# Kernel tuning notes

Hardware: AMD Instinct MI355X
Metric: run time of the kernel (lower is better)

The kernel has to match this reference:

```python
import jax, jax.numpy as jnp
import numpy as np
from jax import lax

B, P, ENC, DEC, ATT, EMB, V, L = 64, 196, 2048, 512, 512, 512, 10000, 30


def setup_inputs() -> dict:
    key = jax.random.key(0)
    ks = jax.random.split(key, 24)
    s = 0.02
    encoder_out = jax.random.normal(ks[0], (B, P, ENC), dtype=jnp.float32)
    encoded_captions = jax.random.randint(ks[1], (B, L), 0, V, dtype=jnp.int64)
    caption_lengths = jax.random.randint(ks[2], (B, 1), 2, L + 1, dtype=jnp.int64)
    # ensure max decode length == L-1 (matches torch max(decode_lengths))
    caption_lengths = caption_lengths.at[0, 0].set(L)
    p = lambda k, sh: jax.random.normal(k, sh, dtype=jnp.float32) * s
    return {
        "encoder_out": encoder_out,
        "encoded_captions": encoded_captions,
        "caption_lengths": caption_lengths,
        "W_enc": p(ks[3], (ATT, ENC)), "b_enc": jnp.zeros((ATT,), jnp.float32),
        "W_dec": p(ks[4], (ATT, DEC)), "b_dec": jnp.zeros((ATT,), jnp.float32),
        "w_full": p(ks[5], (ATT,)), "b_full": jnp.zeros((), jnp.float32),
        "emb_table": jax.random.uniform(ks[6], (V, EMB), jnp.float32, -0.1, 0.1),
        "W_ih": p(ks[7], (4 * DEC, EMB + ENC)), "b_ih": jnp.zeros((4 * DEC,), jnp.float32),
        "W_hh": p(ks[8], (4 * DEC, DEC)), "b_hh": jnp.zeros((4 * DEC,), jnp.float32),
        "W_init_h": p(ks[9], (DEC, ENC)), "b_init_h": jnp.zeros((DEC,), jnp.float32),
        "W_init_c": p(ks[10], (DEC, ENC)), "b_init_c": jnp.zeros((DEC,), jnp.float32),
        "W_beta": p(ks[11], (ENC, DEC)), "b_beta": jnp.zeros((ENC,), jnp.float32),
        "W_fc": jax.random.uniform(ks[12], (V, DEC), jnp.float32, -0.1, 0.1),
        "b_fc": jnp.zeros((V,), jnp.float32),
    }


def reference(encoder_out, encoded_captions, caption_lengths,
              W_enc, b_enc, W_dec, b_dec, w_full, b_full, emb_table,
              W_ih, b_ih, W_hh, b_hh, W_init_h, b_init_h, W_init_c, b_init_c,
              W_beta, b_beta, W_fc, b_fc):
    lengths = caption_lengths[:, 0]
    sort_ind = jnp.argsort(-lengths)  # descending, stable
    enc = encoder_out[sort_ind]            # [B,P,ENC]
    caps = encoded_captions[sort_ind]      # [B,L]
    dec_lens = lengths[sort_ind] - 1       # [B]
    T = caps.shape[1] - 1

    embs = emb_table[caps]                 # [B,L,EMB]
    mean_enc = enc.mean(axis=1)
    h0 = mean_enc @ W_init_h.T + b_init_h
    c0 = mean_enc @ W_init_c.T + b_init_c
    # encoder attention projection is h-independent: compute once
    att1 = jnp.einsum('bpe,ae->bpa', enc, W_enc) + b_enc  # [B,P,ATT]

    def step(carry, xs):
        h, c = carry
        emb_t, mask_t = xs  # [B,EMB], [B] bool
        att2 = h @ W_dec.T + b_dec                              # [B,ATT]
        e = jax.nn.relu(att1 + att2[:, None, :]) @ w_full + b_full  # [B,P]
        alpha = jax.nn.softmax(e, axis=1)
        awe = jnp.einsum('bp,bpe->be', alpha, enc)              # [B,ENC]
        gate = jax.nn.sigmoid(h @ W_beta.T + b_beta)
        awe = gate * awe
        x = jnp.concatenate([emb_t, awe], axis=1)               # [B,EMB+ENC]
        gates = x @ W_ih.T + b_ih + h @ W_hh.T + b_hh           # [B,4D]
        i, f, g, o = jnp.split(gates, 4, axis=1)
        i, f, o = jax.nn.sigmoid(i), jax.nn.sigmoid(f), jax.nn.sigmoid(o)
        g = jnp.tanh(g)
        c_new = f * c + i * g
        h_new = o * jnp.tanh(c_new)
        preds = h_new @ W_fc.T + b_fc                           # [B,V]  (dropout: eval/identity)
        m = mask_t[:, None].astype(preds.dtype)
        return (h_new, c_new), (preds * m, alpha * m)

    mask = jnp.arange(T)[:, None] < dec_lens[None, :]           # [T,B]
    embs_t = jnp.swapaxes(embs[:, :T], 0, 1)                    # [T,B,EMB]
    _, (preds, alphas) = lax.scan(step, (h0, c0), (embs_t, mask))
    predictions = jnp.swapaxes(preds, 0, 1)                     # [B,T,V]
    alphas = jnp.swapaxes(alphas, 0, 1)                         # [B,T,P]
    return predictions, alphas, caps, dec_lens, sort_ind
```

## Files before the change

### kernel.cpp

```cpp
#include <hip/hip_runtime.h>
#include <hip/hip_bf16.h>
#include <math.h>
#include <float.h>

#define BDIM   64
#define PDIM   196
#define ENC    2048
#define DECD   512
#define ATTD   512
#define EMBD   512
#define VOC    10000
#define LCAP   30
#define TSTEPS 29

typedef __attribute__((ext_vector_type(8))) short s8v;
typedef __attribute__((ext_vector_type(4))) float f4v;

__device__ __forceinline__ float sigf(float x) { return 1.0f / (1.0f + expf(-x)); }
__device__ __forceinline__ float bf2f(ushort u) { return __uint_as_float(((uint)u) << 16); }

__global__ void sort_kernel(const int* __restrict__ cap_len,
                            const int* __restrict__ caps,
                            int* __restrict__ sort_ind,
                            int* __restrict__ dec_lens,
                            int* __restrict__ caps_s,
                            float* __restrict__ out_caps,
                            float* __restrict__ out_dlen,
                            float* __restrict__ out_sind) {
    int i = threadIdx.x;
    __shared__ int len[BDIM];
    len[i] = cap_len[i];
    __syncthreads();
    int li = len[i];
    int r = 0;
    for (int j = 0; j < BDIM; ++j) {
        int lj = len[j];
        if (lj > li || (lj == li && j < i)) ++r;
    }
    sort_ind[r] = i;
    dec_lens[r] = li - 1;
    out_sind[r] = (float)i;
    out_dlen[r] = (float)(li - 1);
    for (int tt = 0; tt < LCAP; ++tt) {
        int v = caps[i * LCAP + tt];
        caps_s[r * LCAP + tt] = v;
        out_caps[r * LCAP + tt] = (float)v;
    }
}

__global__ __launch_bounds__(256) void conv_enc_kernel(const float* __restrict__ enc,
                                                       const int* __restrict__ sort_ind,
                                                       __hip_bfloat16* __restrict__ enc_s,
                                                       float* __restrict__ mean_enc) {
    int b = blockIdx.y, tid = threadIdx.x;
    int e = (blockIdx.x << 8) + tid;
    const float* ep = enc + (size_t)sort_ind[b] * (PDIM * ENC) + e;
    __hip_bfloat16* op = enc_s + (size_t)b * (PDIM * ENC) + e;
    float s = 0.f;
    for (int p = 0; p < PDIM; ++p) {
        float v = ep[(size_t)p * ENC];
        s += v;
        op[(size_t)p * ENC] = __float2bfloat16(v);
    }
    mean_enc[(size_t)b * ENC + e] = s * (1.0f / (float)PDIM);
}

__global__ __launch_bounds__(256) void f2b_kernel(const float* __restrict__ src,
                                                  __hip_bfloat16* __restrict__ dst, int n) {
    int i = blockIdx.x * 256 + threadIdx.x;
    if (i < n) dst[i] = __float2bfloat16(src[i]);
}

__global__ __launch_bounds__(256) void h0_kernel(const float* __restrict__ h0f,
                                                 __hip_bfloat16* __restrict__ xh) {
    int idx = blockIdx.x * 256 + threadIdx.x;
    int b = idx >> 9, j = idx & 511;
    xh[(size_t)b * 3072 + 2560 + j] = __float2bfloat16(h0f[idx]);
}

__global__ __launch_bounds__(256) void gemm32_k(
    const float* __restrict__ A, int lda,
    const float* __restrict__ W0, const float* __restrict__ bias0,
    float* __restrict__ C, int ldc, int K) {
    __shared__ float As[16][64];
    __shared__ float Ws[16][64];
    const int tid = threadIdx.x;
    const int tx = tid & 15, ty = tid >> 4;
    const int bn0 = blockIdx.x * 64;
    const int lr = tid >> 2;
    const int lk = (tid & 3) << 2;
    const float* Arow = A + (size_t)lr * lda;
    const int wn = bn0 + lr;
    float acc[4][4];
#pragma unroll
    for (int i = 0; i < 4; ++i)
#pragma unroll
        for (int j = 0; j < 4; ++j) acc[i][j] = 0.f;
    for (int k0 = 0; k0 < K; k0 += 16) {
        float4 av = *(const float4*)(Arow + k0 + lk);
        float4 wv = *(const float4*)(W0 + (size_t)wn * K + k0 + lk);
        __syncthreads();
        As[lk + 0][lr] = av.x; As[lk + 1][lr] = av.y;
        As[lk + 2][lr] = av.z; As[lk + 3][lr] = av.w;
        Ws[lk + 0][lr] = wv.x; Ws[lk + 1][lr] = wv.y;
        Ws[lk + 2][lr] = wv.z; Ws[lk + 3][lr] = wv.w;
        __syncthreads();
#pragma unroll
        for (int kk = 0; kk < 16; ++kk) {
            const float4 a = *(const float4*)&As[kk][ty << 2];
            const float4 w = *(const float4*)&Ws[kk][tx << 2];
            acc[0][0] += a.x * w.x; acc[0][1] += a.x * w.y; acc[0][2] += a.x * w.z; acc[0][3] += a.x * w.w;
            acc[1][0] += a.y * w.x; acc[1][1] += a.y * w.y; acc[1][2] += a.y * w.z; acc[1][3] += a.y * w.w;
            acc[2][0] += a.z * w.x; acc[2][1] += a.z * w.y; acc[2][2] += a.z * w.z; acc[2][3] += a.z * w.w;
            acc[3][0] += a.w * w.x; acc[3][1] += a.w * w.y; acc[3][2] += a.w * w.z; acc[3][3] += a.w * w.w;
        }
    }
#pragma unroll
    for (int i = 0; i < 4; ++i) {
        int row = (ty << 2) + i;
#pragma unroll
        for (int j = 0; j < 4; ++j) {
            int col = bn0 + (tx << 2) + j;
            C[(size_t)row * ldc + col] = acc[i][j] + bias0[col];
        }
    }
}

enum { E_ATT1 = 0, E_GACT = 1, E_GATES = 2, E_PREDS = 3 };

template <int MF, int MODE>
__global__ __launch_bounds__(64) void mfma_gemm(
    const __hip_bfloat16* __restrict__ A, int lda,
    const __hip_bfloat16* __restrict__ W0, const __hip_bfloat16* __restrict__ W1,
    const float* __restrict__ bias0, const float* __restrict__ bias1,
    void* __restrict__ Cv, int K,
    const int* __restrict__ dec_lens, int t) {
    const int l = threadIdx.x;
    const int c16 = l & 15, kg = l >> 4;
    const int n0 = blockIdx.x * 64;
    const int m0 = blockIdx.y * (16 * MF);

    f4v acc[MF][4];
#pragma unroll
    for (int mi = 0; mi < MF; ++mi)
#pragma unroll
        for (int ni = 0; ni < 4; ++ni) acc[mi][ni] = (f4v)0.0f;

    const __hip_bfloat16* arow[MF];
#pragma unroll
    for (int mi = 0; mi < MF; ++mi)
        arow[mi] = A + (size_t)(m0 + mi * 16 + c16) * lda + kg * 8;

    const __hip_bfloat16* wrow[4];
#pragma unroll
    for (int ni = 0; ni < 4; ++ni) {
        int n = n0 + ni * 16 + c16;
        if (MODE == E_GACT)
            wrow[ni] = (n < 2048) ? W0 + (size_t)n * 512 : W1 + (size_t)(n - 2048) * 512;
        else if (MODE == E_GATES)
            wrow[ni] = W0 + (size_t)n * 2560;
        else if (MODE == E_PREDS) {
            int nn = (n < VOC) ? n : (VOC - 1);
            wrow[ni] = W0 + (size_t)nn * K;
        } else
            wrow[ni] = W0 + (size_t)n * K;
        wrow[ni] += kg * 8;
    }

    for (int k0 = 0; k0 < K; k0 += 32) {
        s8v a[MF], b[4];
#pragma unroll
        for (int mi = 0; mi < MF; ++mi)
            a[mi] = *(const s8v*)(arow[mi] + k0);
#pragma unroll
        for (int ni = 0; ni < 4; ++ni) {
            if (MODE == E_GATES && k0 >= 2560)
                b[ni] = *(const s8v*)(W1 + (size_t)(n0 + ni * 16 + c16) * 512 + (k0 - 2560) + kg * 8);
            else
                b[ni] = *(const s8v*)(wrow[ni] + k0);
        }
#pragma unroll
        for (int mi = 0; mi < MF; ++mi)
#pragma unroll
            for (int ni = 0; ni < 4; ++ni)
                acc[mi][ni] = __builtin_amdgcn_mfma_f32_16x16x32_bf16(a[mi], b[ni], acc[mi][ni], 0, 0, 0);
    }

#pragma unroll
    for (int mi = 0; mi < MF; ++mi) {
#pragma unroll
        for (int ni = 0; ni < 4; ++ni) {
#pragma unroll
            for (int i = 0; i < 4; ++i) {
                int r = m0 + mi * 16 + kg * 4 + i;
                int c = n0 + ni * 16 + c16;
                float v = acc[mi][ni][i];
                if (MODE == E_ATT1) {
                    ((__hip_bfloat16*)Cv)[(size_t)r * 512 + c] = __float2bfloat16(v + bias0[c]);
                } else if (MODE == E_GACT) {
                    float* C = (float*)Cv;
                    if (c < 2048) C[(size_t)r * 2560 + c] = sigf(v + bias0[c]);
                    else          C[(size_t)r * 2560 + c] = v + bias1[c - 2048];
                } else if (MODE == E_GATES) {
                    ((float*)Cv)[(size_t)r * 2048 + c] = v + bias0[c] + bias1[c];
                } else {
                    if (c < VOC) {
                        float o = v + bias0[c];
                        ((float*)Cv)[(size_t)r * (TSTEPS * VOC) + (size_t)t * VOC + c] =
                            (t < dec_lens[r]) ? o : 0.f;
                    }
                }
            }
        }
    }
}

__global__ __launch_bounds__(256) void att_kernel(
    const __hip_bfloat16* __restrict__ att1, const float* __restrict__ gact,
    const float* __restrict__ w_full, const float* __restrict__ b_full,
    float* __restrict__ alpha_ws, float* __restrict__ out_alphas,
    const int* __restrict__ dec_lens, int t) {
    int b = blockIdx.x;
    int tid = threadIdx.x;
    __shared__ float s_att2[ATTD];
    __shared__ float s_wf[ATTD];
    __shared__ float s_e[PDIM];
    __shared__ float red[256];

    s_att2[tid]       = gact[(size_t)b * 2560 + 2048 + tid];
    s_att2[tid + 256] = gact[(size_t)b * 2560 + 2048 + 256 + tid];
    s_wf[tid]       = w_full[tid];
    s_wf[tid + 256] = w_full[tid + 256];
    __syncthreads();

    int wv = tid >> 6, lane = tid & 63;
    const float bf = b_full[0];
    const int a0 = lane << 3;
    for (int p = wv; p < PDIM; p += 4) {
        const ushort* row = (const ushort*)att1 + ((size_t)b * PDIM + p) * ATTD + a0;
        float s = 0.f;
#pragma unroll
        for (int i = 0; i < 8; ++i) {
            float x = bf2f(row[i]) + s_att2[a0 + i];
            s += fmaxf(x, 0.f) * s_wf[a0 + i];
        }
#pragma unroll
        for (int off = 32; off; off >>= 1) s += __shfl_xor(s, off);
        if (lane == 0) s_e[p] = s + bf;
    }
    __syncthreads();

    float v = (tid < PDIM) ? s_e[tid] : -FLT_MAX;
    red[tid] = v;
    __syncthreads();
    for (int st = 128; st; st >>= 1) {
        if (tid < st) red[tid] = fmaxf(red[tid], red[tid + st]);
        __syncthreads();
    }
    float mx = red[0];
    __syncthreads();
    float ex = (tid < PDIM) ? expf(v - mx) : 0.f;
    red[tid] = ex;
    __syncthreads();
    for (int st = 128; st; st >>= 1) {
        if (tid < st) red[tid] += red[tid + st];
        __syncthreads();
    }
    float inv = 1.f / red[0];
    if (tid < PDIM) {
        float al = ex * inv;
        alpha_ws[b * PDIM + tid] = al;
        out_alphas[(size_t)b * (TSTEPS * PDIM) + (size_t)t * PDIM + tid] =
            (t < dec_lens[b]) ? al : 0.f;
    }
}

__global__ __launch_bounds__(256) void awe_kernel(
    const __hip_bfloat16* __restrict__ enc_s, const float* __restrict__ alpha_ws,
    const float* __restrict__ gact, const float* __restrict__ emb_table,
    const int* __restrict__ caps_s, __hip_bfloat16* __restrict__ xh, int t) {
    int b = blockIdx.y, tid = threadIdx.x;
    __shared__ float s_al[PDIM];
    if (tid < PDIM) s_al[tid] = alpha_ws[b * PDIM + tid];
    __syncthreads();
    int e = (blockIdx.x << 9) + (tid << 1);
    const ushort* ep = (const ushort*)enc_s + (size_t)b * (PDIM * ENC) + e;
    float a0x = 0.f, a0y = 0.f, a1x = 0.f, a1y = 0.f;
    for (int p = 0; p < PDIM; p += 2) {
        ushort2 u0 = *(const ushort2*)(ep + (size_t)p * ENC);
        ushort2 u1 = *(const ushort2*)(ep + (size_t)(p + 1) * ENC);
        float al0 = s_al[p], al1 = s_al[p + 1];
        a0x += al0 * bf2f(u0.x); a0y += al0 * bf2f(u0.y);
        a1x += al1 * bf2f(u1.x); a1y += al1 * bf2f(u1.y);
    }
    float gx = gact[(size_t)b * 2560 + e];
    float gy = gact[(size_t)b * 2560 + e + 1];
    __hip_bfloat16* xp = xh + (size_t)b * 3072 + 512 + e;
    xp[0] = __float2bfloat16((a0x + a1x) * gx);
    xp[1] = __float2bfloat16((a0y + a1y) * gy);
    if (blockIdx.x == 0) {
        int cap = caps_s[b * LCAP + t];
        int j = tid << 1;
        const float* em = emb_table + (size_t)cap * EMBD + j;
        __hip_bfloat16* xe = xh + (size_t)b * 3072 + j;
        xe[0] = __float2bfloat16(em[0]);
        xe[1] = __float2bfloat16(em[1]);
    }
}

__global__ __launch_bounds__(256) void cell_kernel(const float* __restrict__ gates,
                                                   float* __restrict__ c,
                                                   __hip_bfloat16* __restrict__ xh) {
    int idx = blockIdx.x * 256 + threadIdx.x;
    int b = idx >> 9, j = idx & 511;
    const float* g = gates + (size_t)b * 2048;
    float i_ = sigf(g[j]);
    float f_ = sigf(g[512 + j]);
    float g_ = tanhf(g[1024 + j]);
    float o_ = sigf(g[1536 + j]);
    float cn = f_ * c[idx] + i_ * g_;
    c[idx] = cn;
    xh[(size_t)b * 3072 + 2560 + j] = __float2bfloat16(o_ * tanhf(cn));
}

extern "C" void kernel_launch(void* const* d_in, const int* in_sizes, int n_in,
                              void* d_out, int out_size, void* d_ws, size_t ws_size,
                              hipStream_t stream) {
    const float* enc      = (const float*)d_in[0];
    const int*   caps     = (const int*)d_in[1];
    const int*   clen     = (const int*)d_in[2];
    const float* W_enc    = (const float*)d_in[3];
    const float* b_enc    = (const float*)d_in[4];
    const float* W_dec    = (const float*)d_in[5];
    const float* b_dec    = (const float*)d_in[6];
    const float* w_full   = (const float*)d_in[7];
    const float* b_full   = (const float*)d_in[8];
    const float* emb_tab  = (const float*)d_in[9];
    const float* W_ih     = (const float*)d_in[10];
    const float* b_ih     = (const float*)d_in[11];
    const float* W_hh     = (const float*)d_in[12];
    const float* b_hh     = (const float*)d_in[13];
    const float* W_init_h = (const float*)d_in[14];
    const float* b_init_h = (const float*)d_in[15];
    const float* W_init_c = (const float*)d_in[16];
    const float* b_init_c = (const float*)d_in[17];
    const float* W_beta   = (const float*)d_in[18];
    const float* b_beta   = (const float*)d_in[19];
    const float* W_fc     = (const float*)d_in[20];
    const float* b_fc     = (const float*)d_in[21];

    float* out_pred = (float*)d_out;
    float* out_alph = out_pred + (size_t)BDIM * TSTEPS * VOC;
    float* out_caps = out_alph + (size_t)BDIM * TSTEPS * PDIM;
    float* out_dlen = out_caps + BDIM * LCAP;
    float* out_sind = out_dlen + BDIM;

    char* p = (char*)d_ws;
    auto carve = [&](size_t bytes) { char* r = p; p += (bytes + 255) & ~(size_t)255; return r; };
    int* sort_ind = (int*)carve(64 * 4);
    int* dec_lens = (int*)carve(64 * 4);
    int* caps_s   = (int*)carve(64 * LCAP * 4);
    float* mean_e = (float*)carve((size_t)64 * ENC * 4);
    float* h0f    = (float*)carve((size_t)64 * 512 * 4);
    float* cbuf   = (float*)carve((size_t)64 * 512 * 4);
    float* gact   = (float*)carve((size_t)64 * 2560 * 4);
    float* gates  = (float*)carve((size_t)64 * 2048 * 4);
    float* alpha  = (float*)carve((size_t)64 * PDIM * 4);
    __hip_bfloat16* xh     = (__hip_bfloat16*)carve((size_t)64 * 3072 * 2);
    __hip_bfloat16* enc_s  = (__hip_bfloat16*)carve((size_t)64 * PDIM * ENC * 2);
    __hip_bfloat16* att1   = (__hip_bfloat16*)carve((size_t)64 * PDIM * 512 * 2);
    __hip_bfloat16* Wb_enc = (__hip_bfloat16*)carve((size_t)512 * 2048 * 2);
    __hip_bfloat16* Wb_bet = (__hip_bfloat16*)carve((size_t)2048 * 512 * 2);
    __hip_bfloat16* Wb_dec = (__hip_bfloat16*)carve((size_t)512 * 512 * 2);
    __hip_bfloat16* Wb_ih  = (__hip_bfloat16*)carve((size_t)2048 * 2560 * 2);
    __hip_bfloat16* Wb_hh  = (__hip_bfloat16*)carve((size_t)2048 * 512 * 2);
    __hip_bfloat16* Wb_fc  = (__hip_bfloat16*)carve((size_t)VOC * 512 * 2);

    sort_kernel<<<1, 64, 0, stream>>>(clen, caps, sort_ind, dec_lens, caps_s,
                                      out_caps, out_dlen, out_sind);
    conv_enc_kernel<<<dim3(8, 64), 256, 0, stream>>>(enc, sort_ind, enc_s, mean_e);
    f2b_kernel<<<(512 * 2048 + 255) / 256, 256, 0, stream>>>(W_enc, Wb_enc, 512 * 2048);
    f2b_kernel<<<(2048 * 512 + 255) / 256, 256, 0, stream>>>(W_beta, Wb_bet, 2048 * 512);
    f2b_kernel<<<(512 * 512 + 255) / 256, 256, 0, stream>>>(W_dec, Wb_dec, 512 * 512);
    f2b_kernel<<<(2048 * 2560 + 255) / 256, 256, 0, stream>>>(W_ih, Wb_ih, 2048 * 2560);
    f2b_kernel<<<(2048 * 512 + 255) / 256, 256, 0, stream>>>(W_hh, Wb_hh, 2048 * 512);
    f2b_kernel<<<(VOC * 512 + 255) / 256, 256, 0, stream>>>(W_fc, Wb_fc, VOC * 512);

    gemm32_k<<<dim3(8, 1), 256, 0, stream>>>(mean_e, ENC, W_init_h, b_init_h, h0f, 512, ENC);
    gemm32_k<<<dim3(8, 1), 256, 0, stream>>>(mean_e, ENC, W_init_c, b_init_c, cbuf, 512, ENC);
    h0_kernel<<<128, 256, 0, stream>>>(h0f, xh);

    mfma_gemm<2, E_ATT1><<<dim3(8, 392), 64, 0, stream>>>(
        enc_s, ENC, Wb_enc, nullptr, b_enc, nullptr, att1, ENC, nullptr, 0);

    for (int t = 0; t < TSTEPS; ++t) {
        mfma_gemm<1, E_GACT><<<dim3(40, 4), 64, 0, stream>>>(
            xh + 2560, 3072, Wb_bet, Wb_dec, b_beta, b_dec, gact, 512, nullptr, 0);
        att_kernel<<<64, 256, 0, stream>>>(att1, gact, w_full, b_full,
                                           alpha, out_alph, dec_lens, t);
        awe_kernel<<<dim3(4, 64), 256, 0, stream>>>(enc_s, alpha, gact, emb_tab,
                                                    caps_s, xh, t);
        mfma_gemm<1, E_GATES><<<dim3(32, 4), 64, 0, stream>>>(
            xh, 3072, Wb_ih, Wb_hh, b_ih, b_hh, gates, 3072, nullptr, 0);
        cell_kernel<<<128, 256, 0, stream>>>(gates, cbuf, xh);
        mfma_gemm<1, E_PREDS><<<dim3(157, 4), 64, 0, stream>>>(
            xh + 2560, 3072, Wb_fc, nullptr, b_fc, nullptr, out_pred, 512, dec_lens, t);
    }
}
```

Before: 3.467 ms.

## Fuse attention softmax with weighted encoding and specialize GEMM K at compile time

```diff
diff --git a/kernel.cpp b/kernel.cpp
--- a/kernel.cpp
+++ b/kernel.cpp
@@ -128,17 +128,17 @@
 
 enum { E_ATT1 = 0, E_GACT = 1, E_GATES = 2, E_PREDS = 3 };
 
-template <int MF, int MODE>
+template <int MF, int MODE, int KA, int KB, bool XM>
 __global__ __launch_bounds__(64) void mfma_gemm(
     const __hip_bfloat16* __restrict__ A, int lda,
     const __hip_bfloat16* __restrict__ W0, const __hip_bfloat16* __restrict__ W1,
     const float* __restrict__ bias0, const float* __restrict__ bias1,
-    void* __restrict__ Cv, int K,
+    void* __restrict__ Cv,
     const int* __restrict__ dec_lens, int t) {
     const int l = threadIdx.x;
     const int c16 = l & 15, kg = l >> 4;
-    const int n0 = blockIdx.x * 64;
-    const int m0 = blockIdx.y * (16 * MF);
+    const int n0 = (XM ? (int)blockIdx.y : (int)blockIdx.x) * 64;
+    const int m0 = (XM ? (int)blockIdx.x : (int)blockIdx.y) * (16 * MF);
 
     f4v acc[MF][4];
 #pragma unroll
@@ -151,39 +151,53 @@
     for (int mi = 0; mi < MF; ++mi)
         arow[mi] = A + (size_t)(m0 + mi * 16 + c16) * lda + kg * 8;
 
-    const __hip_bfloat16* wrow[4];
+    const __hip_bfloat16* w0r[4];
+    const __hip_bfloat16* w1r[4];
 #pragma unroll
     for (int ni = 0; ni < 4; ++ni) {
         int n = n0 + ni * 16 + c16;
-        if (MODE == E_GACT)
-            wrow[ni] = (n < 2048) ? W0 + (size_t)n * 512 : W1 + (size_t)(n - 2048) * 512;
-        else if (MODE == E_GATES)
-            wrow[ni] = W0 + (size_t)n * 2560;
-        else if (MODE == E_PREDS) {
+        if (MODE == E_GACT) {
+            w0r[ni] = (n < 2048) ? W0 + (size_t)n * 512 : W1 + (size_t)(n - 2048) * 512;
+        } else if (MODE == E_GATES) {
+            w0r[ni] = W0 + (size_t)n * (KA);
+            w1r[ni] = W1 + (size_t)n * (KB);
+        } else if (MODE == E_PREDS) {
             int nn = (n < VOC) ? n : (VOC - 1);
-            wrow[ni] = W0 + (size_t)nn * K;
-        } else
-            wrow[ni] = W0 + (size_t)n * K;
-        wrow[ni] += kg * 8;
-    }
-
-    for (int k0 = 0; k0 < K; k0 += 32) {
+            w0r[ni] = W0 + (size_t)nn * KA;
+        } else {
+            w0r[ni] = W0 + (size_t)n * KA;
+        }
+        w0r[ni] += kg * 8;
+        if (MODE == E_GATES) w1r[ni] += kg * 8;
+    }
+
+#pragma unroll 8
+    for (int k0 = 0; k0 < KA; k0 += 32) {
         s8v a[MF], b[4];
 #pragma unroll
-        for (int mi = 0; mi < MF; ++mi)
-            a[mi] = *(const s8v*)(arow[mi] + k0);
-#pragma unroll
-        for (int ni = 0; ni < 4; ++ni) {
-            if (MODE == E_GATES && k0 >= 2560)
-                b[ni] = *(const s8v*)(W1 + (size_t)(n0 + ni * 16 + c16) * 512 + (k0 - 2560) + kg * 8);
-            else
-                b[ni] = *(const s8v*)(wrow[ni] + k0);
-        }
+        for (int mi = 0; mi < MF; ++mi) a[mi] = *(const s8v*)(arow[mi] + k0);
+#pragma unroll
+        for (int ni = 0; ni < 4; ++ni) b[ni] = *(const s8v*)(w0r[ni] + k0);
 #pragma unroll
         for (int mi = 0; mi < MF; ++mi)
 #pragma unroll
             for (int ni = 0; ni < 4; ++ni)
                 acc[mi][ni] = __builtin_amdgcn_mfma_f32_16x16x32_bf16(a[mi], b[ni], acc[mi][ni], 0, 0, 0);
+    }
+    if constexpr (KB > 0) {
+#pragma unroll
+        for (int k0 = 0; k0 < KB; k0 += 32) {
+            s8v a[MF], b[4];
+#pragma unroll
+            for (int mi = 0; mi < MF; ++mi) a[mi] = *(const s8v*)(arow[mi] + KA + k0);
+#pragma unroll
+            for (int ni = 0; ni < 4; ++ni) b[ni] = *(const s8v*)(w1r[ni] + k0);
+#pragma unroll
+            for (int mi = 0; mi < MF; ++mi)
+#pragma unroll
+                for (int ni = 0; ni < 4; ++ni)
+                    acc[mi][ni] = __builtin_amdgcn_mfma_f32_16x16x32_bf16(a[mi], b[ni], acc[mi][ni], 0, 0, 0);
+        }
     }
 
 #pragma unroll
@@ -215,11 +229,13 @@
     }
 }
 
-__global__ __launch_bounds__(256) void att_kernel(
+__global__ __launch_bounds__(256) void attawe_kernel(
     const __hip_bfloat16* __restrict__ att1, const float* __restrict__ gact,
+    const __hip_bfloat16* __restrict__ enc_s,
     const float* __restrict__ w_full, const float* __restrict__ b_full,
-    float* __restrict__ alpha_ws, float* __restrict__ out_alphas,
-    const int* __restrict__ dec_lens, int t) {
+    const float* __restrict__ emb_table,
+    const int* __restrict__ caps_s, const int* __restrict__ dec_lens,
+    __hip_bfloat16* __restrict__ xh, float* __restrict__ out_alphas, int t) {
     int b = blockIdx.x;
     int tid = threadIdx.x;
     __shared__ float s_att2[ATTD];
@@ -267,44 +283,44 @@
         __syncthreads();
     }
     float inv = 1.f / red[0];
+    __syncthreads();
     if (tid < PDIM) {
         float al = ex * inv;
-        alpha_ws[b * PDIM + tid] = al;
+        s_e[tid] = al;
         out_alphas[(size_t)b * (TSTEPS * PDIM) + (size_t)t * PDIM + tid] =
             (t < dec_lens[b]) ? al : 0.f;
     }
-}
-
-__global__ __launch_bounds__(256) void awe_kernel(
-    const __hip_bfloat16* __restrict__ enc_s, const float* __restrict__ alpha_ws,
-    const float* __restrict__ gact, const float* __restrict__ emb_table,
-    const int* __restrict__ caps_s, __hip_bfloat16* __restrict__ xh, int t) {
-    int b = blockIdx.y, tid = threadIdx.x;
-    __shared__ float s_al[PDIM];
-    if (tid < PDIM) s_al[tid] = alpha_ws[b * PDIM + tid];
-    __syncthreads();
-    int e = (blockIdx.x << 9) + (tid << 1);
+    __syncthreads();
+
+    int e = tid << 3;
     const ushort* ep = (const ushort*)enc_s + (size_t)b * (PDIM * ENC) + e;
-    float a0x = 0.f, a0y = 0.f, a1x = 0.f, a1y = 0.f;
-    for (int p = 0; p < PDIM; p += 2) {
-        ushort2 u0 = *(const ushort2*)(ep + (size_t)p * ENC);
-        ushort2 u1 = *(const ushort2*)(ep + (size_t)(p + 1) * ENC);
-        float al0 = s_al[p], al1 = s_al[p + 1];
-        a0x += al0 * bf2f(u0.x); a0y += al0 * bf2f(u0.y);
-        a1x += al1 * bf2f(u1.x); a1y += al1 * bf2f(u1.y);
-    }
-    float gx = gact[(size_t)b * 2560 + e];
-    float gy = gact[(size_t)b * 2560 + e + 1];
-    __hip_bfloat16* xp = xh + (size_t)b * 3072 + 512 + e;
-    xp[0] = __float2bfloat16((a0x + a1x) * gx);
-    xp[1] = __float2bfloat16((a0y + a1y) * gy);
-    if (blockIdx.x == 0) {
+    float acc[8];
+#pragma unroll
+    for (int i = 0; i < 8; ++i) acc[i] = 0.f;
+#pragma unroll 2
+    for (int p = 0; p < PDIM; ++p) {
+        float al = s_e[p];
+        s8v u = *(const s8v*)(ep + (size_t)p * ENC);
+#pragma unroll
+        for (int i = 0; i < 8; ++i) acc[i] += al * bf2f((ushort)u[i]);
+    }
+    float4 g0 = *(const float4*)(gact + (size_t)b * 2560 + e);
+    float4 g1 = *(const float4*)(gact + (size_t)b * 2560 + e + 4);
+    __hip_bfloat16 ob[8];
+    ob[0] = __float2bfloat16(acc[0] * g0.x); ob[1] = __float2bfloat16(acc[1] * g0.y);
+    ob[2] = __float2bfloat16(acc[2] * g0.z); ob[3] = __float2bfloat16(acc[3] * g0.w);
+    ob[4] = __float2bfloat16(acc[4] * g1.x); ob[5] = __float2bfloat16(acc[5] * g1.y);
+    ob[6] = __float2bfloat16(acc[6] * g1.z); ob[7] = __float2bfloat16(acc[7] * g1.w);
+    *(uint4*)(xh + (size_t)b * 3072 + 512 + e) = *(uint4*)ob;
+
+    if (tid < 128) {
         int cap = caps_s[b * LCAP + t];
-        int j = tid << 1;
-        const float* em = emb_table + (size_t)cap * EMBD + j;
-        __hip_bfloat16* xe = xh + (size_t)b * 3072 + j;
-        xe[0] = __float2bfloat16(em[0]);
-        xe[1] = __float2bfloat16(em[1]);
+        int j = tid << 2;
+        float4 em = *(const float4*)(emb_table + (size_t)cap * EMBD + j);
+        __hip_bfloat16 eb[4];
+        eb[0] = __float2bfloat16(em.x); eb[1] = __float2bfloat16(em.y);
+        eb[2] = __float2bfloat16(em.z); eb[3] = __float2bfloat16(em.w);
+        *(uint2*)(xh + (size_t)b * 3072 + j) = *(uint2*)eb;
     }
 }
 
@@ -365,7 +381,6 @@
     float* cbuf   = (float*)carve((size_t)64 * 512 * 4);
     float* gact   = (float*)carve((size_t)64 * 2560 * 4);
     float* gates  = (float*)carve((size_t)64 * 2048 * 4);
-    float* alpha  = (float*)carve((size_t)64 * PDIM * 4);
     __hip_bfloat16* xh     = (__hip_bfloat16*)carve((size_t)64 * 3072 * 2);
     __hip_bfloat16* enc_s  = (__hip_bfloat16*)carve((size_t)64 * PDIM * ENC * 2);
     __hip_bfloat16* att1   = (__hip_bfloat16*)carve((size_t)64 * PDIM * 512 * 2);
@@ -390,20 +405,19 @@
     gemm32_k<<<dim3(8, 1), 256, 0, stream>>>(mean_e, ENC, W_init_c, b_init_c, cbuf, 512, ENC);
     h0_kernel<<<128, 256, 0, stream>>>(h0f, xh);
 
-    mfma_gemm<2, E_ATT1><<<dim3(8, 392), 64, 0, stream>>>(
-        enc_s, ENC, Wb_enc, nullptr, b_enc, nullptr, att1, ENC, nullptr, 0);
+    mfma_gemm<2, E_ATT1, 2048, 0, true><<<dim3(392, 8), 64, 0, stream>>>(
+        enc_s, ENC, Wb_enc, nullptr, b_enc, nullptr, att1, nullptr, 0);
 
     for (int t = 0; t < TSTEPS; ++t) {
-        mfma_gemm<1, E_GACT><<<dim3(40, 4), 64, 0, stream>>>(
-            xh + 2560, 3072, Wb_bet, Wb_dec, b_beta, b_dec, gact, 512, nullptr, 0);
-        att_kernel<<<64, 256, 0, stream>>>(att1, gact, w_full, b_full,
-                                           alpha, out_alph, dec_lens, t);
-        awe_kernel<<<dim3(4, 64), 256, 0, stream>>>(enc_s, alpha, gact, emb_tab,
-                                                    caps_s, xh, t);
-        mfma_gemm<1, E_GATES><<<dim3(32, 4), 64, 0, stream>>>(
-            xh, 3072, Wb_ih, Wb_hh, b_ih, b_hh, gates, 3072, nullptr, 0);
+        mfma_gemm<1, E_GACT, 512, 0, false><<<dim3(40, 4), 64, 0, stream>>>(
+            xh + 2560, 3072, Wb_bet, Wb_dec, b_beta, b_dec, gact, nullptr, 0);
+        attawe_kernel<<<64, 256, 0, stream>>>(att1, gact, enc_s, w_full, b_full,
+                                              emb_tab, caps_s, dec_lens, xh,
+                                              out_alph, t);
+        mfma_gemm<1, E_GATES, 2560, 512, false><<<dim3(32, 4), 64, 0, stream>>>(
+            xh, 3072, Wb_ih, Wb_hh, b_ih, b_hh, gates, nullptr, 0);
         cell_kernel<<<128, 256, 0, stream>>>(gates, cbuf, xh);
-        mfma_gemm<1, E_PREDS><<<dim3(157, 4), 64, 0, stream>>>(
-            xh + 2560, 3072, Wb_fc, nullptr, b_fc, nullptr, out_pred, 512, dec_lens, t);
-    }
-}
+        mfma_gemm<1, E_PREDS, 512, 0, false><<<dim3(160, 4), 64, 0, stream>>>(
+            xh + 2560, 3072, Wb_fc, nullptr, b_fc, nullptr, out_pred, dec_lens, t);
+    }
+}
```

Measured after the change: 3.655 ms. 1.05x slower.
